# Kernel tuning notes

Hardware: AMD Instinct MI355X
Metric: run time of the kernel (lower is better)

The kernel has to match this reference:

```python
import jax, jax.numpy as jnp
import numpy as np

D_MODEL = 256
N_HEADS = 8
D_K = D_MODEL // N_HEADS


def setup_inputs() -> dict:
    key = jax.random.key(0)
    ks = jax.random.split(key, 9)
    s = 1.0 / np.sqrt(D_MODEL)
    x = jax.random.normal(ks[0], (2, 4096, D_MODEL), dtype=jnp.float32)
    Wq = jax.random.uniform(ks[1], (D_MODEL, D_MODEL), minval=-s, maxval=s)
    bq = jax.random.uniform(ks[2], (D_MODEL,), minval=-s, maxval=s)
    Wk = jax.random.uniform(ks[3], (D_MODEL, D_MODEL), minval=-s, maxval=s)
    bk = jax.random.uniform(ks[4], (D_MODEL,), minval=-s, maxval=s)
    Wv = jax.random.uniform(ks[5], (D_MODEL, D_MODEL), minval=-s, maxval=s)
    bv = jax.random.uniform(ks[6], (D_MODEL,), minval=-s, maxval=s)
    Wo = jax.random.uniform(ks[7], (D_MODEL, D_MODEL), minval=-s, maxval=s)
    bo = jax.random.uniform(ks[8], (D_MODEL,), minval=-s, maxval=s)
    return {"q": x, "Wq": Wq, "bq": bq, "Wk": Wk, "bk": bk,
            "Wv": Wv, "bv": bv, "Wo": Wo, "bo": bo}


def reference(q, Wq, bq, Wk, bk, Wv, bv, Wo, bo):
    B, L, _ = q.shape
    # nn.Linear: y = x @ W.T + b ; weights stored as [out, in]
    Q = (jnp.einsum('bld,ed->ble', q, Wq) + bq).reshape(B, L, N_HEADS, D_K).transpose(0, 2, 1, 3)
    K = (jnp.einsum('bld,ed->ble', q, Wk) + bk).reshape(B, L, N_HEADS, D_K).transpose(0, 2, 1, 3)
    V = (jnp.einsum('bld,ed->ble', q, Wv) + bv).reshape(B, L, N_HEADS, D_K).transpose(0, 2, 1, 3)
    scores = jnp.einsum('bhqd,bhkd->bhqk', Q, K) / jnp.sqrt(jnp.float32(D_K))
    attn = jax.nn.softmax(scores, axis=-1)  # dropout p=0 (eval): identity
    out = jnp.einsum('bhqk,bhkd->bhqd', attn, V)
    out = out.transpose(0, 2, 1, 3).reshape(B, L, D_MODEL)
    return jnp.einsum('bld,ed->ble', out, Wo) + bo
```

## Files before the change

kernel.cpp:

```cpp
#include <hip/hip_runtime.h>

#define D_MODEL 256
#define NH 8
#define DK 32
#define SEQ 4096
#define BATCH 2
#define M_ROWS (BATCH * SEQ)
#define QSCALE 0.17677669529663687f

typedef __attribute__((ext_vector_type(8))) short bf16x8;
typedef __attribute__((ext_vector_type(4))) short s16x4;
typedef __attribute__((ext_vector_type(4))) float f32x4;
typedef __attribute__((ext_vector_type(16))) float f32x16;

static __device__ __forceinline__ short f2bf(float f) {
    unsigned u = __float_as_uint(f);
    u += 0x7fff + ((u >> 16) & 1);
    return (short)(u >> 16);
}

__global__ void cvt_all(const float* __restrict__ x, short* __restrict__ xb,
                        const float* __restrict__ W0, const float* __restrict__ W1,
                        const float* __restrict__ W2, const float* __restrict__ W3,
                        short* __restrict__ D0, short* __restrict__ D1,
                        short* __restrict__ D2, short* __restrict__ D3) {
    const int blk = blockIdx.x;
    const float* s;
    short* d;
    int i;
    if (blk < 2048) {
        s = x; d = xb; i = blk * blockDim.x + threadIdx.x;
    } else {
        const int seg = (blk - 2048) >> 6;
        i = ((blk - 2048) & 63) * blockDim.x + threadIdx.x;
        s = seg == 0 ? W0 : seg == 1 ? W1 : seg == 2 ? W2 : W3;
        d = seg == 0 ? D0 : seg == 1 ? D1 : seg == 2 ? D2 : D3;
    }
    float4 v = reinterpret_cast<const float4*>(s)[i];
    s16x4 o;
    o.x = f2bf(v.x); o.y = f2bf(v.y); o.z = f2bf(v.z); o.w = f2bf(v.w);
    reinterpret_cast<s16x4*>(d)[i] = o;
}

__global__ __launch_bounds__(256) void qkv_gemm(
    const short* __restrict__ A,
    const short* __restrict__ Wqb, const short* __restrict__ Wkb, const short* __restrict__ Wvb,
    const float* __restrict__ bq, const float* __restrict__ bk, const float* __restrict__ bv,
    short* __restrict__ Qb, short* __restrict__ Kblk, short* __restrict__ Vblk)
{
    const int ct = blockIdx.x;
    const int rt = blockIdx.y;
    const int tid = threadIdx.x;
    const int w = tid >> 6, l = tid & 63, l15 = l & 15, g = l >> 4;
    const int mat = ct >> 2;
    const int colbase = (ct & 3) * 64;
    const short* W = mat == 0 ? Wqb : mat == 1 ? Wkb : Wvb;
    const float* bias = mat == 0 ? bq : mat == 1 ? bk : bv;

    const int arow = rt * 64 + w * 16 + l15;
    f32x4 acc[4] = {};
#pragma unroll
    for (int ks = 0; ks < 8; ++ks) {
        bf16x8 af = *reinterpret_cast<const bf16x8*>(&A[(size_t)arow * 256 + ks * 32 + 8 * g]);
#pragma unroll
        for (int c = 0; c < 4; ++c) {
            const int col = colbase + 16 * c + l15;
            bf16x8 wf = *reinterpret_cast<const bf16x8*>(&W[(size_t)col * 256 + ks * 32 + 8 * g]);
            acc[c] = __builtin_amdgcn_mfma_f32_16x16x32_bf16(af, wf, acc[c], 0, 0, 0);
        }
    }

#pragma unroll
    for (int c = 0; c < 4; ++c) {
        const int col = colbase + 16 * c + l15;
        const float bv_ = bias[col];
#pragma unroll
        for (int r = 0; r < 4; ++r) {
            const int m = rt * 64 + w * 16 + 4 * g + r;
            const float v = acc[c][r] + bv_;
            const int head = col >> 5, d = col & 31;
            const int bb = m >> 12, seq = m & 4095;
            const size_t bhbase = (size_t)(bb * NH + head) * (SEQ * DK);
            if (mat == 0) {
                Qb[bhbase + (size_t)seq * 32 + d] = f2bf(v * QSCALE);
            } else if (mat == 1) {
                const int t = seq >> 6, s = (seq >> 5) & 1, lk = seq & 31;
                const int hh = (d >> 4) & 1, gk = (d >> 3) & 1, jk = d & 7;
                Kblk[bhbase + t * 2048 + (s * 2 + hh) * 512 + (gk * 32 + lk) * 8 + jk] = f2bf(v);
            } else {
                const int t = seq >> 6, w6 = seq & 63;
                const int c2 = w6 >> 4, gv = (w6 >> 2) & 1, jv = ((w6 >> 3) & 1) * 4 + (w6 & 3);
                Vblk[bhbase + t * 2048 + c2 * 512 + (gv * 32 + d) * 8 + jv] = f2bf(v);
            }
        }
    }
}

__global__ __launch_bounds__(256, 4) void attn_kernel(
    const short* __restrict__ Qb, const short* __restrict__ Kblk,
    const short* __restrict__ Vblk, short* __restrict__ AOb)
{
    __shared__ float accL[3][64][17];

    const int bid = ((int)blockIdx.x & 7) * 256 + ((int)blockIdx.x >> 3);
    const int qt = bid & 127;
    const int bh = bid >> 7;
    const int b = bh >> 3, h = bh & 7;
    const int w = threadIdx.x >> 6;
    const int l = threadIdx.x & 63;
    const int l31 = l & 31, g1 = l >> 5;

    const short* Qh = Qb + (size_t)bh * (SEQ * DK);
    const int q0 = qt * 32;
    const bf16x8 qf0 = *(const bf16x8*)&Qh[(size_t)(q0 + l31) * 32 + g1 * 8];
    const bf16x8 qf1 = *(const bf16x8*)&Qh[(size_t)(q0 + l31) * 32 + 16 + g1 * 8];

    const char* Kt = (const char*)Kblk + (size_t)bh * 262144 + (size_t)w * 65536 + l * 16;
    const char* Vt = (const char*)Vblk + (size_t)bh * 262144 + (size_t)w * 65536 + l * 16;

    f32x16 acc;
#pragma unroll
    for (int r = 0; r < 16; ++r) acc[r] = 0.f;
    f32x16 Z0;
#pragma unroll
    for (int r = 0; r < 16; ++r) Z0[r] = 0.f;
    float ls0 = 0.f, ls1 = 0.f, ls2 = 0.f, ls3 = 0.f;

    auto loadt = [&](bf16x8& K0, bf16x8& K1, bf16x8& K2, bf16x8& K3,
                     bf16x8& V0, bf16x8& V1, bf16x8& V2, bf16x8& V3, int tl) {
        const char* kp = Kt + (size_t)tl * 4096;
        const char* vp = Vt + (size_t)tl * 4096;
        K0 = *(const bf16x8*)(kp);        K1 = *(const bf16x8*)(kp + 1024);
        K2 = *(const bf16x8*)(kp + 2048); K3 = *(const bf16x8*)(kp + 3072);
        V0 = *(const bf16x8*)(vp);        V1 = *(const bf16x8*)(vp + 1024);
        V2 = *(const bf16x8*)(vp + 2048); V3 = *(const bf16x8*)(vp + 3072);
    };

    auto compute = [&](const bf16x8& K0, const bf16x8& K1, const bf16x8& K2, const bf16x8& K3,
                       const bf16x8& V0, const bf16x8& V1, const bf16x8& V2, const bf16x8& V3) {
        union { unsigned u[16]; bf16x8 v[4]; } P;
#pragma unroll
        for (int s = 0; s < 2; ++s) {
            f32x16 z = __builtin_amdgcn_mfma_f32_32x32x16_bf16(s ? K3 : K1, qf1, Z0, 0, 0, 0);
            z = __builtin_amdgcn_mfma_f32_32x32x16_bf16(s ? K2 : K0, qf0, z, 0, 0, 0);
            float e[16];
#pragma unroll
            for (int r = 0; r < 16; ++r) e[r] = __expf(z[r]);
#pragma unroll
            for (int r = 0; r < 16; r += 4) {
                ls0 += e[r]; ls1 += e[r + 1]; ls2 += e[r + 2]; ls3 += e[r + 3];
            }
#pragma unroll
            for (int i = 0; i < 8; ++i)
                asm("v_cvt_pk_bf16_f32 %0, %1, %2" : "=v"(P.u[s * 8 + i]) : "v"(e[2 * i]), "v"(e[2 * i + 1]));
        }
#pragma unroll
        for (int c = 0; c < 4; ++c) {
            const bf16x8& vf = (c == 0) ? V0 : (c == 1) ? V1 : (c == 2) ? V2 : V3;
            acc = __builtin_amdgcn_mfma_f32_32x32x16_bf16(P.v[c], vf, acc, 0, 0, 0);
        }
    };

    bf16x8 kA0, kA1, kA2, kA3, vA0, vA1, vA2, vA3;
    bf16x8 kB0, kB1, kB2, kB3, vB0, vB1, vB2, vB3;
    loadt(kA0, kA1, kA2, kA3, vA0, vA1, vA2, vA3, 0);
    for (int i = 0; i < 8; ++i) {
        loadt(kB0, kB1, kB2, kB3, vB0, vB1, vB2, vB3, 2 * i + 1);
        compute(kA0, kA1, kA2, kA3, vA0, vA1, vA2, vA3);
        if (i < 7) loadt(kA0, kA1, kA2, kA3, vA0, vA1, vA2, vA3, 2 * i + 2);
        compute(kB0, kB1, kB2, kB3, vB0, vB1, vB2, vB3);
    }

    float ls = (ls0 + ls1) + (ls2 + ls3);
    ls += __shfl_xor(ls, 32);

    if (w > 0) {
#pragma unroll
        for (int r = 0; r < 16; ++r) accL[w - 1][l][r] = acc[r];
        accL[w - 1][l][16] = ls;
    }
    __syncthreads();
    if (w == 0) {
#pragma unroll
        for (int wv = 0; wv < 3; ++wv) {
#pragma unroll
            for (int r = 0; r < 16; ++r) acc[r] += accL[wv][l][r];
            ls += accL[wv][l][16];
        }
        const float inv = 1.0f / ls;
#pragma unroll
        for (int r = 0; r < 16; ++r) {
            const int ql = (r & 3) + 8 * (r >> 2) + 4 * g1;
            const float invq = __shfl(inv, ql);
            AOb[((size_t)b * SEQ + q0 + ql) * D_MODEL + h * DK + l31] = f2bf(acc[r] * invq);
        }
    }
}

__global__ __launch_bounds__(256) void out_gemm(
    const short* __restrict__ AOb, const short* __restrict__ Wob,
    const float* __restrict__ bo, float* __restrict__ out)
{
    const int ct = blockIdx.x, rt = blockIdx.y;
    const int tid = threadIdx.x;
    const int w = tid >> 6, l = tid & 63, l15 = l & 15, g = l >> 4;
    const int arow = rt * 64 + w * 16 + l15;

    f32x4 acc[4] = {};
#pragma unroll
    for (int ks = 0; ks < 8; ++ks) {
        bf16x8 af = *(const bf16x8*)&AOb[(size_t)arow * 256 + ks * 32 + 8 * g];
#pragma unroll
        for (int c = 0; c < 4; ++c) {
            const int col = ct * 64 + 16 * c + l15;
            bf16x8 wf = *(const bf16x8*)&Wob[(size_t)col * 256 + ks * 32 + 8 * g];
            acc[c] = __builtin_amdgcn_mfma_f32_16x16x32_bf16(af, wf, acc[c], 0, 0, 0);
        }
    }
#pragma unroll
    for (int c = 0; c < 4; ++c) {
        const int col = ct * 64 + 16 * c + l15;
        const float bv_ = bo[col];
#pragma unroll
        for (int r = 0; r < 4; ++r) {
            const int m = rt * 64 + w * 16 + 4 * g + r;
            out[(size_t)m * 256 + col] = acc[c][r] + bv_;
        }
    }
}

extern "C" void kernel_launch(void* const* d_in, const int* in_sizes, int n_in,
                              void* d_out, int out_size, void* d_ws, size_t ws_size,
                              hipStream_t stream) {
    const float* x  = (const float*)d_in[0];
    const float* Wq = (const float*)d_in[1];
    const float* bq = (const float*)d_in[2];
    const float* Wk = (const float*)d_in[3];
    const float* bk = (const float*)d_in[4];
    const float* Wv = (const float*)d_in[5];
    const float* bv = (const float*)d_in[6];
    const float* Wo = (const float*)d_in[7];
    const float* bo = (const float*)d_in[8];
    float* out = (float*)d_out;

    char* ws = (char*)d_ws;
    const size_t MB = 1 << 20, KB = 1 << 10;
    short* xb   = (short*)(ws);
    short* Wqb  = (short*)(ws + 4 * MB);
    short* Wkb  = (short*)(ws + 4 * MB + 128 * KB);
    short* Wvb  = (short*)(ws + 4 * MB + 256 * KB);
    short* Wob  = (short*)(ws + 4 * MB + 384 * KB);
    short* Qb   = (short*)(ws + 4 * MB + 512 * KB);
    short* Kblk = (short*)(ws + 8 * MB + 512 * KB);
    short* Vblk = (short*)(ws + 12 * MB + 512 * KB);
    short* AOb  = (short*)(ws + 16 * MB + 512 * KB);

    cvt_all<<<2304, 256, 0, stream>>>(x, xb, Wq, Wk, Wv, Wo, Wqb, Wkb, Wvb, Wob);

    dim3 gq(12, 128);
    qkv_gemm<<<gq, 256, 0, stream>>>(xb, Wqb, Wkb, Wvb, bq, bk, bv, Qb, Kblk, Vblk);

    attn_kernel<<<2048, 256, 0, stream>>>(Qb, Kblk, Vblk, AOb);

    dim3 go(4, 128);
    out_gemm<<<go, 256, 0, stream>>>(AOb, Wob, bo, out);
}
```

Baseline: 111.7 us.

## Process two 32-row query tiles per attention block to reuse K/V loads

Each attention block now handles 64 query rows as two 32-row sub-tiles, so every K/V fragment loaded from global memory feeds twice the MFMA work, and the grid is halved. The explicit double-buffered register prefetch of K/V tiles is dropped in favour of a simple loop, and the occupancy hint in launch_bounds is removed. This trades higher register and LDS use, plus fewer blocks, for half the K/V traffic; load latency hiding now depends on the compiler and on the interleaving of the two sub-tiles.

```diff
diff --git a/kernel.cpp b/kernel.cpp
--- a/kernel.cpp
+++ b/kernel.cpp
@@ -96,103 +96,117 @@
     }
 }
 
-__global__ __launch_bounds__(256, 4) void attn_kernel(
+__global__ __launch_bounds__(256) void attn_kernel(
     const short* __restrict__ Qb, const short* __restrict__ Kblk,
     const short* __restrict__ Vblk, short* __restrict__ AOb)
 {
-    __shared__ float accL[3][64][17];
-
-    const int bid = ((int)blockIdx.x & 7) * 256 + ((int)blockIdx.x >> 3);
-    const int qt = bid & 127;
-    const int bh = bid >> 7;
+    __shared__ float accL[3][64][35];
+
+    const int bid = ((int)blockIdx.x & 7) * 128 + ((int)blockIdx.x >> 3);
+    const int qt = bid & 63;
+    const int bh = bid >> 6;
     const int b = bh >> 3, h = bh & 7;
     const int w = threadIdx.x >> 6;
     const int l = threadIdx.x & 63;
     const int l31 = l & 31, g1 = l >> 5;
 
     const short* Qh = Qb + (size_t)bh * (SEQ * DK);
-    const int q0 = qt * 32;
-    const bf16x8 qf0 = *(const bf16x8*)&Qh[(size_t)(q0 + l31) * 32 + g1 * 8];
-    const bf16x8 qf1 = *(const bf16x8*)&Qh[(size_t)(q0 + l31) * 32 + 16 + g1 * 8];
+    const int q0 = qt * 64;
+    const bf16x8 qfA0 = *(const bf16x8*)&Qh[(size_t)(q0 + l31) * 32 + g1 * 8];
+    const bf16x8 qfA1 = *(const bf16x8*)&Qh[(size_t)(q0 + l31) * 32 + 16 + g1 * 8];
+    const bf16x8 qfB0 = *(const bf16x8*)&Qh[(size_t)(q0 + 32 + l31) * 32 + g1 * 8];
+    const bf16x8 qfB1 = *(const bf16x8*)&Qh[(size_t)(q0 + 32 + l31) * 32 + 16 + g1 * 8];
 
     const char* Kt = (const char*)Kblk + (size_t)bh * 262144 + (size_t)w * 65536 + l * 16;
     const char* Vt = (const char*)Vblk + (size_t)bh * 262144 + (size_t)w * 65536 + l * 16;
 
-    f32x16 acc;
-#pragma unroll
-    for (int r = 0; r < 16; ++r) acc[r] = 0.f;
-    f32x16 Z0;
-#pragma unroll
-    for (int r = 0; r < 16; ++r) Z0[r] = 0.f;
-    float ls0 = 0.f, ls1 = 0.f, ls2 = 0.f, ls3 = 0.f;
-
-    auto loadt = [&](bf16x8& K0, bf16x8& K1, bf16x8& K2, bf16x8& K3,
-                     bf16x8& V0, bf16x8& V1, bf16x8& V2, bf16x8& V3, int tl) {
-        const char* kp = Kt + (size_t)tl * 4096;
-        const char* vp = Vt + (size_t)tl * 4096;
-        K0 = *(const bf16x8*)(kp);        K1 = *(const bf16x8*)(kp + 1024);
-        K2 = *(const bf16x8*)(kp + 2048); K3 = *(const bf16x8*)(kp + 3072);
-        V0 = *(const bf16x8*)(vp);        V1 = *(const bf16x8*)(vp + 1024);
-        V2 = *(const bf16x8*)(vp + 2048); V3 = *(const bf16x8*)(vp + 3072);
-    };
-
-    auto compute = [&](const bf16x8& K0, const bf16x8& K1, const bf16x8& K2, const bf16x8& K3,
-                       const bf16x8& V0, const bf16x8& V1, const bf16x8& V2, const bf16x8& V3) {
-        union { unsigned u[16]; bf16x8 v[4]; } P;
+    f32x16 accA, accB;
+#pragma unroll
+    for (int r = 0; r < 16; ++r) { accA[r] = 0.f; accB[r] = 0.f; }
+    float lsA0 = 0.f, lsA1 = 0.f, lsA2 = 0.f, lsA3 = 0.f;
+    float lsB0 = 0.f, lsB1 = 0.f, lsB2 = 0.f, lsB3 = 0.f;
+
+    for (int t = 0; t < 16; ++t) {
+        const char* kp = Kt + (size_t)t * 4096;
+        const char* vp = Vt + (size_t)t * 4096;
+        bf16x8 K0 = *(const bf16x8*)(kp);        bf16x8 K1 = *(const bf16x8*)(kp + 1024);
+        bf16x8 K2 = *(const bf16x8*)(kp + 2048); bf16x8 K3 = *(const bf16x8*)(kp + 3072);
+        bf16x8 V0 = *(const bf16x8*)(vp);        bf16x8 V1 = *(const bf16x8*)(vp + 1024);
+        bf16x8 V2 = *(const bf16x8*)(vp + 2048); bf16x8 V3 = *(const bf16x8*)(vp + 3072);
+
 #pragma unroll
         for (int s = 0; s < 2; ++s) {
-            f32x16 z = __builtin_amdgcn_mfma_f32_32x32x16_bf16(s ? K3 : K1, qf1, Z0, 0, 0, 0);
-            z = __builtin_amdgcn_mfma_f32_32x32x16_bf16(s ? K2 : K0, qf0, z, 0, 0, 0);
-            float e[16];
-#pragma unroll
-            for (int r = 0; r < 16; ++r) e[r] = __expf(z[r]);
-#pragma unroll
-            for (int r = 0; r < 16; r += 4) {
-                ls0 += e[r]; ls1 += e[r + 1]; ls2 += e[r + 2]; ls3 += e[r + 3];
+            const bf16x8 Ka = s ? K2 : K0, Kb = s ? K3 : K1;
+            const bf16x8 Vc0 = s ? V2 : V0, Vc1 = s ? V3 : V1;
+            f32x16 zz;
+#pragma unroll
+            for (int r = 0; r < 16; ++r) zz[r] = 0.f;
+            {
+                f32x16 z = __builtin_amdgcn_mfma_f32_32x32x16_bf16(Kb, qfA1, zz, 0, 0, 0);
+                z = __builtin_amdgcn_mfma_f32_32x32x16_bf16(Ka, qfA0, z, 0, 0, 0);
+                float e[16];
+#pragma unroll
+                for (int r = 0; r < 16; ++r) e[r] = __expf(z[r]);
+#pragma unroll
+                for (int r = 0; r < 16; r += 4) {
+                    lsA0 += e[r]; lsA1 += e[r + 1]; lsA2 += e[r + 2]; lsA3 += e[r + 3];
+                }
+                union { unsigned u[8]; bf16x8 v[2]; } pk;
+#pragma unroll
+                for (int i = 0; i < 8; ++i)
+                    asm("v_cvt_pk_bf16_f32 %0, %1, %2" : "=v"(pk.u[i]) : "v"(e[2 * i]), "v"(e[2 * i + 1]));
+                accA = __builtin_amdgcn_mfma_f32_32x32x16_bf16(pk.v[0], Vc0, accA, 0, 0, 0);
+                accA = __builtin_amdgcn_mfma_f32_32x32x16_bf16(pk.v[1], Vc1, accA, 0, 0, 0);
             }
-#pragma unroll
-            for (int i = 0; i < 8; ++i)
-                asm("v_cvt_pk_bf16_f32 %0, %1, %2" : "=v"(P.u[s * 8 + i]) : "v"(e[2 * i]), "v"(e[2 * i + 1]));
-        }
-#pragma unroll
-        for (int c = 0; c < 4; ++c) {
-            const bf16x8& vf = (c == 0) ? V0 : (c == 1) ? V1 : (c == 2) ? V2 : V3;
-            acc = __builtin_amdgcn_mfma_f32_32x32x16_bf16(P.v[c], vf, acc, 0, 0, 0);
-        }
-    };
-
-    bf16x8 kA0, kA1, kA2, kA3, vA0, vA1, vA2, vA3;
-    bf16x8 kB0, kB1, kB2, kB3, vB0, vB1, vB2, vB3;
-    loadt(kA0, kA1, kA2, kA3, vA0, vA1, vA2, vA3, 0);
-    for (int i = 0; i < 8; ++i) {
-        loadt(kB0, kB1, kB2, kB3, vB0, vB1, vB2, vB3, 2 * i + 1);
-        compute(kA0, kA1, kA2, kA3, vA0, vA1, vA2, vA3);
-        if (i < 7) loadt(kA0, kA1, kA2, kA3, vA0, vA1, vA2, vA3, 2 * i + 2);
-        compute(kB0, kB1, kB2, kB3, vB0, vB1, vB2, vB3);
-    }
-
-    float ls = (ls0 + ls1) + (ls2 + ls3);
-    ls += __shfl_xor(ls, 32);
+            {
+                f32x16 z = __builtin_amdgcn_mfma_f32_32x32x16_bf16(Kb, qfB1, zz, 0, 0, 0);
+                z = __builtin_amdgcn_mfma_f32_32x32x16_bf16(Ka, qfB0, z, 0, 0, 0);
+                float e[16];
+#pragma unroll
+                for (int r = 0; r < 16; ++r) e[r] = __expf(z[r]);
+#pragma unroll
+                for (int r = 0; r < 16; r += 4) {
+                    lsB0 += e[r]; lsB1 += e[r + 1]; lsB2 += e[r + 2]; lsB3 += e[r + 3];
+                }
+                union { unsigned u[8]; bf16x8 v[2]; } pk;
+#pragma unroll
+                for (int i = 0; i < 8; ++i)
+                    asm("v_cvt_pk_bf16_f32 %0, %1, %2" : "=v"(pk.u[i]) : "v"(e[2 * i]), "v"(e[2 * i + 1]));
+                accB = __builtin_amdgcn_mfma_f32_32x32x16_bf16(pk.v[0], Vc0, accB, 0, 0, 0);
+                accB = __builtin_amdgcn_mfma_f32_32x32x16_bf16(pk.v[1], Vc1, accB, 0, 0, 0);
+            }
+        }
+    }
+
+    float lsA = (lsA0 + lsA1) + (lsA2 + lsA3);
+    float lsB = (lsB0 + lsB1) + (lsB2 + lsB3);
+    lsA += __shfl_xor(lsA, 32);
+    lsB += __shfl_xor(lsB, 32);
 
     if (w > 0) {
 #pragma unroll
-        for (int r = 0; r < 16; ++r) accL[w - 1][l][r] = acc[r];
-        accL[w - 1][l][16] = ls;
+        for (int r = 0; r < 16; ++r) { accL[w - 1][l][r] = accA[r]; accL[w - 1][l][16 + r] = accB[r]; }
+        accL[w - 1][l][32] = lsA;
+        accL[w - 1][l][33] = lsB;
     }
     __syncthreads();
     if (w == 0) {
 #pragma unroll
         for (int wv = 0; wv < 3; ++wv) {
 #pragma unroll
-            for (int r = 0; r < 16; ++r) acc[r] += accL[wv][l][r];
-            ls += accL[wv][l][16];
-        }
-        const float inv = 1.0f / ls;
+            for (int r = 0; r < 16; ++r) { accA[r] += accL[wv][l][r]; accB[r] += accL[wv][l][16 + r]; }
+            lsA += accL[wv][l][32];
+            lsB += accL[wv][l][33];
+        }
+        const float invA = 1.0f / lsA;
+        const float invB = 1.0f / lsB;
 #pragma unroll
         for (int r = 0; r < 16; ++r) {
             const int ql = (r & 3) + 8 * (r >> 2) + 4 * g1;
-            const float invq = __shfl(inv, ql);
-            AOb[((size_t)b * SEQ + q0 + ql) * D_MODEL + h * DK + l31] = f2bf(acc[r] * invq);
+            const float iA = __shfl(invA, ql);
+            const float iB = __shfl(invB, ql);
+            AOb[((size_t)b * SEQ + q0 + ql) * D_MODEL + h * DK + l31] = f2bf(accA[r] * iA);
+            AOb[((size_t)b * SEQ + q0 + 32 + ql) * D_MODEL + h * DK + l31] = f2bf(accB[r] * iB);
         }
     }
 }
@@ -260,7 +274,7 @@
     dim3 gq(12, 128);
     qkv_gemm<<<gq, 256, 0, stream>>>(xb, Wqb, Wkb, Wvb, bq, bk, bv, Qb, Kblk, Vblk);
 
-    attn_kernel<<<2048, 256, 0, stream>>>(Qb, Kblk, Vblk, AOb);
+    attn_kernel<<<1024, 256, 0, stream>>>(Qb, Kblk, Vblk, AOb);
 
     dim3 go(4, 128);
     out_gemm<<<go, 256, 0, stream>>>(AOb, Wob, bo, out);
```

New measurement: 110.2 us. No clear change (-1.4%).

## Replace manual double-buffered K/V prefetch with simple loop and interleaved PV MFMAs

Applied to the files above, without the earlier changes.

Removes the explicit A/B register double-buffering of K/V tiles and replaces it with a plain 16-iteration loop that loads each tile and computes on it. The PV MFMAs are now issued right after each half's softmax packing instead of after both halves, the persistent zero accumulator register is dropped, and the occupancy hint is removed from launch bounds. The aim is lower register pressure and letting the compiler schedule loads. The cost is that explicit software prefetch is lost, so global load latency may be less hidden.

```diff
diff --git a/kernel.cpp b/kernel.cpp
--- a/kernel.cpp
+++ b/kernel.cpp
@@ -96,7 +96,7 @@
     }
 }
 
-__global__ __launch_bounds__(256, 4) void attn_kernel(
+__global__ __launch_bounds__(256) void attn_kernel(
     const short* __restrict__ Qb, const short* __restrict__ Kblk,
     const short* __restrict__ Vblk, short* __restrict__ AOb)
 {
@@ -121,27 +121,22 @@
     f32x16 acc;
 #pragma unroll
     for (int r = 0; r < 16; ++r) acc[r] = 0.f;
-    f32x16 Z0;
-#pragma unroll
-    for (int r = 0; r < 16; ++r) Z0[r] = 0.f;
     float ls0 = 0.f, ls1 = 0.f, ls2 = 0.f, ls3 = 0.f;
 
-    auto loadt = [&](bf16x8& K0, bf16x8& K1, bf16x8& K2, bf16x8& K3,
-                     bf16x8& V0, bf16x8& V1, bf16x8& V2, bf16x8& V3, int tl) {
-        const char* kp = Kt + (size_t)tl * 4096;
-        const char* vp = Vt + (size_t)tl * 4096;
-        K0 = *(const bf16x8*)(kp);        K1 = *(const bf16x8*)(kp + 1024);
-        K2 = *(const bf16x8*)(kp + 2048); K3 = *(const bf16x8*)(kp + 3072);
-        V0 = *(const bf16x8*)(vp);        V1 = *(const bf16x8*)(vp + 1024);
-        V2 = *(const bf16x8*)(vp + 2048); V3 = *(const bf16x8*)(vp + 3072);
-    };
-
-    auto compute = [&](const bf16x8& K0, const bf16x8& K1, const bf16x8& K2, const bf16x8& K3,
-                       const bf16x8& V0, const bf16x8& V1, const bf16x8& V2, const bf16x8& V3) {
-        union { unsigned u[16]; bf16x8 v[4]; } P;
+    for (int t = 0; t < 16; ++t) {
+        const char* kp = Kt + (size_t)t * 4096;
+        const char* vp = Vt + (size_t)t * 4096;
+        bf16x8 K0 = *(const bf16x8*)(kp);        bf16x8 K1 = *(const bf16x8*)(kp + 1024);
+        bf16x8 K2 = *(const bf16x8*)(kp + 2048); bf16x8 K3 = *(const bf16x8*)(kp + 3072);
+        bf16x8 V0 = *(const bf16x8*)(vp);        bf16x8 V1 = *(const bf16x8*)(vp + 1024);
+        bf16x8 V2 = *(const bf16x8*)(vp + 2048); bf16x8 V3 = *(const bf16x8*)(vp + 3072);
+
 #pragma unroll
         for (int s = 0; s < 2; ++s) {
-            f32x16 z = __builtin_amdgcn_mfma_f32_32x32x16_bf16(s ? K3 : K1, qf1, Z0, 0, 0, 0);
+            f32x16 zz;
+#pragma unroll
+            for (int r = 0; r < 16; ++r) zz[r] = 0.f;
+            f32x16 z = __builtin_amdgcn_mfma_f32_32x32x16_bf16(s ? K3 : K1, qf1, zz, 0, 0, 0);
             z = __builtin_amdgcn_mfma_f32_32x32x16_bf16(s ? K2 : K0, qf0, z, 0, 0, 0);
             float e[16];
 #pragma unroll
@@ -150,25 +145,13 @@
             for (int r = 0; r < 16; r += 4) {
                 ls0 += e[r]; ls1 += e[r + 1]; ls2 += e[r + 2]; ls3 += e[r + 3];
             }
+            union { unsigned u[8]; bf16x8 v[2]; } pk;
 #pragma unroll
             for (int i = 0; i < 8; ++i)
-                asm("v_cvt_pk_bf16_f32 %0, %1, %2" : "=v"(P.u[s * 8 + i]) : "v"(e[2 * i]), "v"(e[2 * i + 1]));
-        }
-#pragma unroll
-        for (int c = 0; c < 4; ++c) {
-            const bf16x8& vf = (c == 0) ? V0 : (c == 1) ? V1 : (c == 2) ? V2 : V3;
-            acc = __builtin_amdgcn_mfma_f32_32x32x16_bf16(P.v[c], vf, acc, 0, 0, 0);
-        }
-    };
-
-    bf16x8 kA0, kA1, kA2, kA3, vA0, vA1, vA2, vA3;
-    bf16x8 kB0, kB1, kB2, kB3, vB0, vB1, vB2, vB3;
-    loadt(kA0, kA1, kA2, kA3, vA0, vA1, vA2, vA3, 0);
-    for (int i = 0; i < 8; ++i) {
-        loadt(kB0, kB1, kB2, kB3, vB0, vB1, vB2, vB3, 2 * i + 1);
-        compute(kA0, kA1, kA2, kA3, vA0, vA1, vA2, vA3);
-        if (i < 7) loadt(kA0, kA1, kA2, kA3, vA0, vA1, vA2, vA3, 2 * i + 2);
-        compute(kB0, kB1, kB2, kB3, vB0, vB1, vB2, vB3);
+                asm("v_cvt_pk_bf16_f32 %0, %1, %2" : "=v"(pk.u[i]) : "v"(e[2 * i]), "v"(e[2 * i + 1]));
+            acc = __builtin_amdgcn_mfma_f32_32x32x16_bf16(pk.v[0], s ? V2 : V0, acc, 0, 0, 0);
+            acc = __builtin_amdgcn_mfma_f32_32x32x16_bf16(pk.v[1], s ? V3 : V1, acc, 0, 0, 0);
+        }
     }
 
     float ls = (ls0 + ls1) + (ls2 + ls3);
```

New measurement: 115.3 us. 1.03x slower.
